# Kernel optimization log

Hardware: AMD Instinct MI355X
Metric: run time of the kernel (lower is better)

The kernel has to match this reference:

```python
import jax, jax.numpy as jnp
import numpy as np

T, B, E, H = 2048, 2, 1024, 16
Dh = E // H


def setup_inputs() -> dict:
    key = jax.random.key(0)
    ks = jax.random.split(key, 5)
    s = 0.02
    query = jax.random.normal(ks[0], (T, B, E), dtype=jnp.float32)
    Wq = jax.random.normal(ks[1], (E, E), dtype=jnp.float32) * s
    Wk = jax.random.normal(ks[2], (E, E), dtype=jnp.float32) * s
    Wv = jax.random.normal(ks[3], (E, E), dtype=jnp.float32) * s
    Wo = jax.random.normal(ks[4], (E, E), dtype=jnp.float32) * s
    bq = jnp.zeros((E,), jnp.float32)
    bk = jnp.zeros((E,), jnp.float32)
    bv = jnp.zeros((E,), jnp.float32)
    bo = jnp.zeros((E,), jnp.float32)
    # additive causal mask: 0 on/below diagonal, -inf above (standard fairseq usage)
    neg = jnp.finfo(jnp.float32).min
    attn_mask = jnp.where(jnp.triu(jnp.ones((T, T), jnp.bool_), k=1), neg, 0.0).astype(jnp.float32)
    return {"query": query, "Wq": Wq, "bq": bq, "Wk": Wk, "bk": bk,
            "Wv": Wv, "bv": bv, "Wo": Wo, "bo": bo, "attn_mask": attn_mask}


def reference(query, Wq, bq, Wk, bk, Wv, bv, Wo, bo, attn_mask):
    t, b, e = query.shape
    scale = Dh ** -0.5
    # self-attention projections (nn.Linear: x @ W.T + b)
    q = (query @ Wq.T + bq) * scale  # [T,B,E]
    k = query @ Wk.T + bk
    v = query @ Wv.T + bv
    # [T, B*H, Dh] -> [B*H, T, Dh]
    q = q.reshape(t, b * H, Dh).transpose(1, 0, 2)
    k = k.reshape(t, b * H, Dh).transpose(1, 0, 2)
    v = v.reshape(t, b * H, Dh).transpose(1, 0, 2)
    # explicit bmm -> softmax -> bmm (materializes [B*H, T, T])
    attn_weights = jnp.einsum('btd,bsd->bts', q, k) + attn_mask[None, :, :]
    attn_probs = jax.nn.softmax(attn_weights, axis=-1)
    attn = jnp.einsum('bts,bsd->btd', attn_probs, v)  # [B*H, T, Dh]
    attn = attn.transpose(1, 0, 2).reshape(t, b, e)  # [T,B,E]
    out = attn @ Wo.T + bo
    return out
```

## Files before the change

kernel.cpp:

```cpp
#include <hip/hip_runtime.h>


typedef __attribute__((ext_vector_type(8))) short   s16x8;
typedef __attribute__((ext_vector_type(4))) float   f32x4;
typedef __attribute__((ext_vector_type(2))) __fp16  f16x2;
typedef __attribute__((ext_vector_type(4))) __fp16  f16x4;

#define MFMA16(a, b, c) __builtin_amdgcn_mfma_f32_16x16x32_bf16((a), (b), (c), 0, 0, 0)
#define MFMApv(a, b, c) __builtin_amdgcn_mfma_f32_16x16x16f16((a), (b), (c), 0, 0, 0)

static __device__ __forceinline__ unsigned short f2bf(float f) {
    unsigned u = __float_as_uint(f);
    unsigned r = u + 0x7fffu + ((u >> 16) & 1u);
    return (unsigned short)(r >> 16);
}

static __device__ __forceinline__ void gl2lds16(const void* g, void* l) {
    __builtin_amdgcn_global_load_lds(
        (const __attribute__((address_space(1))) unsigned int*)g,
        (__attribute__((address_space(3))) unsigned int*)l, 16, 0, 0);
}

__global__ __launch_bounds__(256) void cvt_all(const float* __restrict__ query,
                                               const float* __restrict__ w0,
                                               const float* __restrict__ w1,
                                               const float* __restrict__ w2,
                                               const float* __restrict__ w3,
                                               unsigned short* __restrict__ Xb,
                                               unsigned short* __restrict__ Wcat) {
    const int bx = blockIdx.x;
    if (bx < 4096) {
        const int i = threadIdx.x;
        const float4 f = reinterpret_cast<const float4*>(query + (size_t)bx * 1024)[i];
        ushort4 u;
        u.x = f2bf(f.x); u.y = f2bf(f.y); u.z = f2bf(f.z); u.w = f2bf(f.w);
        const int mrow = (bx & 1) * 2048 + (bx >> 1);
        reinterpret_cast<ushort4*>(Xb + (size_t)mrow * 1024)[i] = u;
    } else {
        const int j   = bx - 4096;
        const int sel = j >> 10;
        const int i   = (j & 1023) * 256 + threadIdx.x;
        const float* src = (sel == 0) ? w0 : (sel == 1) ? w1 : (sel == 2) ? w2 : w3;
        const float4 f = reinterpret_cast<const float4*>(src)[i];
        ushort4 u;
        u.x = f2bf(f.x); u.y = f2bf(f.y); u.z = f2bf(f.z); u.w = f2bf(f.w);
        reinterpret_cast<ushort4*>(Wcat + (size_t)sel * 1048576)[i] = u;
    }
}

__global__ __launch_bounds__(256) void gemm_qkv(const unsigned short* __restrict__ A,
                                                const unsigned short* __restrict__ W,
                                                const float* __restrict__ b0,
                                                const float* __restrict__ b1,
                                                const float* __restrict__ b2,
                                                unsigned short* __restrict__ outQK,
                                                __fp16* __restrict__ outV) {
    __shared__ __align__(16) unsigned short smem[16384];
    unsigned short* Al = smem;
    unsigned short* Bl = smem + 8192;

    const int tid  = threadIdx.x;
    const int w    = tid >> 6;
    const int lane = tid & 63;
    const int quad = lane >> 4;
    const int c    = lane & 15;
    const int wm   = w >> 1;
    const int wn   = w & 1;

    const int id   = blockIdx.x;
    const int xcd  = id & 7;
    const int slot = id >> 3;
    const int m0 = (xcd * 4 + (slot & 3)) * 128;
    const int n0 = (slot >> 2) * 128;

    f32x4 acc[4][4];
    #pragma unroll
    for (int mi = 0; mi < 4; ++mi)
        #pragma unroll
        for (int ni = 0; ni < 4; ++ni) acc[mi][ni] = (f32x4){0.f, 0.f, 0.f, 0.f};

    const int srow = tid >> 3;
    const int g    = (tid & 7) ^ (srow & 7);
    const unsigned short* aG = A + (size_t)(m0 + srow) * 1024 + g * 8;
    const unsigned short* wG = W + (size_t)(n0 + srow) * 1024 + g * 8;
    const int loff = tid * 8;

    const int cs = (c & 7);

    for (int kk = 0; kk < 16; ++kk) {
        const int k0 = kk * 64;
        __syncthreads();
        #pragma unroll
        for (int i = 0; i < 4; ++i) {
            gl2lds16(aG + k0 + i * 32 * 1024, &Al[loff + i * 2048]);
            gl2lds16(wG + k0 + i * 32 * 1024, &Bl[loff + i * 2048]);
        }
        __syncthreads();

        s16x8 af[4][2], bf[4][2];
        #pragma unroll
        for (int mi = 0; mi < 4; ++mi) {
            const int row = (wm * 64 + mi * 16 + c) * 64;
            af[mi][0] = *reinterpret_cast<const s16x8*>(&Al[row + ((quad ^ cs) << 3)]);
            af[mi][1] = *reinterpret_cast<const s16x8*>(&Al[row + (((4 + quad) ^ cs) << 3)]);
        }
        #pragma unroll
        for (int ni = 0; ni < 4; ++ni) {
            const int row = (wn * 64 + ni * 16 + c) * 64;
            bf[ni][0] = *reinterpret_cast<const s16x8*>(&Bl[row + ((quad ^ cs) << 3)]);
            bf[ni][1] = *reinterpret_cast<const s16x8*>(&Bl[row + (((4 + quad) ^ cs) << 3)]);
        }
        #pragma unroll
        for (int mi = 0; mi < 4; ++mi)
            #pragma unroll
            for (int ni = 0; ni < 4; ++ni) {
                acc[mi][ni] = MFMA16(af[mi][0], bf[ni][0], acc[mi][ni]);
                acc[mi][ni] = MFMA16(af[mi][1], bf[ni][1], acc[mi][ni]);
            }
    }

    const int sel = n0 >> 10;
    if (sel < 2) {
        const float scale = (sel == 0) ? 0.18033688011112042f : 1.0f;
        const float* bias = (sel == 0) ? b0 : b1;
        #pragma unroll
        for (int ni = 0; ni < 4; ++ni) {
            const int n = n0 + wn * 64 + ni * 16 + c;
            const float bval = bias[n & 1023];
            #pragma unroll
            for (int mi = 0; mi < 4; ++mi)
                #pragma unroll
                for (int r = 0; r < 4; ++r) {
                    const int m = m0 + wm * 64 + mi * 16 + quad * 4 + r;
                    outQK[(size_t)m * 2048 + n] = f2bf((acc[mi][ni][r] + bval) * scale);
                }
        }
    } else {
        __syncthreads();
        #pragma unroll
        for (int ni = 0; ni < 4; ++ni) {
            const int n = wn * 64 + ni * 16 + c;
            const float bval = b2[(n0 - 2048) + n];
            #pragma unroll
            for (int mi = 0; mi < 4; ++mi) {
                const int m = wm * 64 + mi * 16 + quad * 4;
                const f16x2 lo = __builtin_amdgcn_cvt_pkrtz(acc[mi][ni][0] + bval,
                                                            acc[mi][ni][1] + bval);
                const f16x2 hi = __builtin_amdgcn_cvt_pkrtz(acc[mi][ni][2] + bval,
                                                            acc[mi][ni][3] + bval);
                uint2 st;
                st.x = __builtin_bit_cast(unsigned int, lo);
                st.y = __builtin_bit_cast(unsigned int, hi);
                const int phys = n * 128 + (((m >> 3) ^ (n & 15)) << 3) + (m & 7);
                *reinterpret_cast<uint2*>(&smem[phys]) = st;
            }
        }
        __syncthreads();
        const int n = tid >> 1;
        const int vcol = (n0 - 2048) + n;
        const int bb = m0 >> 11, tbase = m0 & 2047;
        __fp16* vdst = outV + ((size_t)((bb * 16 + (vcol >> 6)) * 64 + (vcol & 63))) * 2048 + tbase;
        #pragma unroll
        for (int j = 0; j < 8; ++j) {
            const int lc = (tid & 1) * 8 + j;
            const int phys = n * 128 + ((lc ^ (n & 15)) << 3);
            *reinterpret_cast<uint4*>(vdst + lc * 8) =
                *reinterpret_cast<const uint4*>(&smem[phys]);
        }
    }
}

__global__ __launch_bounds__(256) void gemm_out(const unsigned short* __restrict__ A,
                                                const unsigned short* __restrict__ W,
                                                const float* __restrict__ bias,
                                                float* __restrict__ outF) {
    __shared__ __align__(16) unsigned short Al[64 * 64];
    __shared__ __align__(16) unsigned short Bl[128 * 64];

    const int tid  = threadIdx.x;
    const int w    = tid >> 6;
    const int lane = tid & 63;
    const int quad = lane >> 4;
    const int c    = lane & 15;

    const int id   = blockIdx.x;
    const int xcd  = id & 7;
    const int slot = id >> 3;
    const int m0 = (xcd * 8 + (slot & 7)) * 64;
    const int n0 = (slot >> 3) * 128;

    f32x4 acc[8];
    #pragma unroll
    for (int ni = 0; ni < 8; ++ni) acc[ni] = (f32x4){0.f, 0.f, 0.f, 0.f};

    const int srow = tid >> 3;
    const int g    = (tid & 7) ^ (srow & 7);
    const unsigned short* aG = A + (size_t)(m0 + srow) * 1024 + g * 8;
    const unsigned short* wG = W + (size_t)(n0 + srow) * 1024 + g * 8;
    const int loff = tid * 8;

    const int cs = (c & 7);

    for (int kk = 0; kk < 16; ++kk) {
        const int k0 = kk * 64;
        __syncthreads();
        gl2lds16(aG + k0,             &Al[loff]);
        gl2lds16(aG + k0 + 32 * 1024, &Al[loff + 2048]);
        #pragma unroll
        for (int i = 0; i < 4; ++i)
            gl2lds16(wG + k0 + i * 32 * 1024, &Bl[loff + i * 2048]);
        __syncthreads();

        const int arow = (w * 16 + c) * 64;
        const s16x8 af0 = *reinterpret_cast<const s16x8*>(&Al[arow + ((quad ^ cs) << 3)]);
        const s16x8 af1 = *reinterpret_cast<const s16x8*>(&Al[arow + (((4 + quad) ^ cs) << 3)]);
        #pragma unroll
        for (int ni = 0; ni < 8; ++ni) {
            const int brow = (ni * 16 + c) * 64;
            const s16x8 bf0 = *reinterpret_cast<const s16x8*>(&Bl[brow + ((quad ^ cs) << 3)]);
            const s16x8 bf1 = *reinterpret_cast<const s16x8*>(&Bl[brow + (((4 + quad) ^ cs) << 3)]);
            acc[ni] = MFMA16(af0, bf0, acc[ni]);
            acc[ni] = MFMA16(af1, bf1, acc[ni]);
        }
    }

    #pragma unroll
    for (int ni = 0; ni < 8; ++ni) {
        const int n = n0 + ni * 16 + c;
        const float bval = bias[n];
        const int m = m0 + w * 16 + quad * 4;
        const int bb = m >> 11, t = m & 2047;
        #pragma unroll
        for (int r = 0; r < 4; ++r)
            outF[(size_t)(2 * (t + r) + bb) * 1024 + n] = acc[ni][r] + bval;
    }
}

__global__ __launch_bounds__(256, 4) void attn_kernel(const unsigned short* __restrict__ QKb,
                                                      const __fp16* __restrict__ Vt,
                                                      unsigned short* __restrict__ Ob) {
    __shared__ unsigned short Kl[2][2][64][32];
    __shared__ __fp16 Vl[2][64][64];

    const int tid  = threadIdx.x;
    const int w    = tid >> 6;
    const int lane = tid & 63;
    const int quad = lane >> 4;
    const int c    = lane & 15;

    const int id = blockIdx.x;
    const int bh = (id & 7) * 4 + ((id >> 3) & 3);
    const int a  = 31 - (id >> 5);
    const int bB = bh >> 4, h = bh & 15;
    const int t0 = a * 64;
    const int trg = t0 + w * 16;
    const int nIt = a + 1;

    const unsigned short* qp = QKb + (size_t)(bB * 2048 + trg + c) * 2048 + h * 64 + quad * 8;
    const s16x8 aq0 = *reinterpret_cast<const s16x8*>(qp);
    const s16x8 aq1 = *reinterpret_cast<const s16x8*>(qp + 32);

    const int lr4 = lane >> 2, sl4 = lane & 3;
    const unsigned short* kSrc = QKb + (size_t)(bB * 2048 + w * 16 + lr4) * 2048
                                 + 1024 + h * 64 + (sl4 ^ ((lane >> 3) & 3)) * 8;
    const int vr8 = lane >> 3, sl8 = lane & 7;
    const __fp16* vSrcA = Vt + (size_t)(bh * 64 + w * 16 + vr8) * 2048 + (sl8 ^ vr8) * 8;
    const __fp16* vSrcB = vSrcA + (size_t)8 * 2048;

    f32x4 acc[4];
    float l = 0.f;
    #pragma unroll
    for (int dt = 0; dt < 4; ++dt) acc[dt] = (f32x4){0.f, 0.f, 0.f, 0.f};

    const int kswz = (quad ^ ((c >> 1) & 3)) * 8;

    {
        gl2lds16(kSrc,      &Kl[0][0][w * 16 + lr4][sl4 * 8]);
        gl2lds16(kSrc + 32, &Kl[0][1][w * 16 + lr4][sl4 * 8]);
        gl2lds16(vSrcA,     &Vl[0][w * 16 + vr8][sl8 * 8]);
        gl2lds16(vSrcB,     &Vl[0][w * 16 + 8 + vr8][sl8 * 8]);
    }

    for (int it = 0; it < nIt; ++it) {
        const int buf = it & 1;
        __syncthreads();
        if (it + 1 < nIt) {
            const size_t s1 = (size_t)(it + 1) * 64;
            const int nb = buf ^ 1;
            gl2lds16(kSrc + s1 * 2048,      &Kl[nb][0][w * 16 + lr4][sl4 * 8]);
            gl2lds16(kSrc + s1 * 2048 + 32, &Kl[nb][1][w * 16 + lr4][sl4 * 8]);
            gl2lds16(vSrcA + s1,            &Vl[nb][w * 16 + vr8][sl8 * 8]);
            gl2lds16(vSrcB + s1,            &Vl[nb][w * 16 + 8 + vr8][sl8 * 8]);
        }

        s16x8 kf[4][2];
        #pragma unroll
        for (int ns = 0; ns < 4; ++ns) {
            kf[ns][0] = *reinterpret_cast<const s16x8*>(&Kl[buf][0][ns * 16 + c][kswz]);
            kf[ns][1] = *reinterpret_cast<const s16x8*>(&Kl[buf][1][ns * 16 + c][kswz]);
        }
        f16x4 vf[4][4];
        #pragma unroll
        for (int dt = 0; dt < 4; ++dt)
            #pragma unroll
            for (int ch = 0; ch < 4; ++ch) {
                const int phys = ((2 * ch + (quad >> 1)) ^ (c & 7)) * 8 + (quad & 1) * 4;
                vf[dt][ch] = *reinterpret_cast<const f16x4*>(&Vl[buf][dt * 16 + c][phys]);
            }

        const int s0 = it * 64;
        const bool diag = (it == a);
        f32x4 sT[4];
        #pragma unroll
        for (int ns = 0; ns < 4; ++ns) {
            f32x4 z = (f32x4){0.f, 0.f, 0.f, 0.f};
            z = MFMA16(kf[ns][0], aq0, z);
            sT[ns] = MFMA16(kf[ns][1], aq1, z);
        }
        f16x4 pf[4];
        float lp = 0.f;
        #pragma unroll
        for (int ns = 0; ns < 4; ++ns) {
            float pv[4];
            #pragma unroll
            for (int r = 0; r < 4; ++r) pv[r] = exp2f(sT[ns][r]);
            if (diag) {
                const int sb = s0 + ns * 16 + quad * 4;
                const int qg = trg + c;
                #pragma unroll
                for (int r = 0; r < 4; ++r) if (sb + r > qg) pv[r] = 0.f;
            }
            lp += (pv[0] + pv[1]) + (pv[2] + pv[3]);
            const f16x2 lo = __builtin_amdgcn_cvt_pkrtz(pv[0], pv[1]);
            const f16x2 hi = __builtin_amdgcn_cvt_pkrtz(pv[2], pv[3]);
            pf[ns] = __builtin_shufflevector(lo, hi, 0, 1, 2, 3);
        }
        l += lp;
        #pragma unroll
        for (int dt = 0; dt < 4; ++dt)
            #pragma unroll
            for (int ns = 0; ns < 4; ++ns)
                acc[dt] = MFMApv(vf[dt][ns], pf[ns], acc[dt]);
    }

    float lv = l;
    lv += __shfl_xor(lv, 16);
    lv += __shfl_xor(lv, 32);
    const float inv = 1.0f / lv;
    const size_t base = (size_t)(bB * 2048 + trg + c) * 1024 + h * 64;
    #pragma unroll
    for (int dt = 0; dt < 4; ++dt) {
        const unsigned u0 = (unsigned)f2bf(acc[dt][0] * inv)
                          | ((unsigned)f2bf(acc[dt][1] * inv) << 16);
        const unsigned u1 = (unsigned)f2bf(acc[dt][2] * inv)
                          | ((unsigned)f2bf(acc[dt][3] * inv) << 16);
        uint2 st; st.x = u0; st.y = u1;
        *reinterpret_cast<uint2*>(Ob + base + dt * 16 + quad * 4) = st;
    }
}

extern "C" void kernel_launch(void* const* d_in, const int* in_sizes, int n_in,
                              void* d_out, int out_size, void* d_ws, size_t ws_size,
                              hipStream_t stream) {
    const float* query = (const float*)d_in[0];
    const float* Wq    = (const float*)d_in[1];
    const float* bq    = (const float*)d_in[2];
    const float* Wk    = (const float*)d_in[3];
    const float* bk    = (const float*)d_in[4];
    const float* Wv    = (const float*)d_in[5];
    const float* bv    = (const float*)d_in[6];
    const float* Wo    = (const float*)d_in[7];
    const float* bo    = (const float*)d_in[8];

    float* out = (float*)d_out;

    unsigned short* ws    = (unsigned short*)d_ws;
    unsigned short* Xbf   = ws;
    unsigned short* Wcat  = Xbf  + (size_t)4096 * 1024;
    unsigned short* QKb   = Wcat + (size_t)4 * 1024 * 1024;
    __fp16*         Vtw   = (__fp16*)(QKb + (size_t)4096 * 2048);
    unsigned short* attnb = (unsigned short*)(Vtw + (size_t)32 * 64 * 2048);

    cvt_all<<<8192, 256, 0, stream>>>(query, Wq, Wk, Wv, Wo, Xbf, Wcat);

    gemm_qkv<<<768, 256, 0, stream>>>(Xbf, Wcat, bq, bk, bv, QKb, Vtw);

    attn_kernel<<<1024, 256, 0, stream>>>(QKb, Vtw, attnb);

    gemm_out<<<512, 256, 0, stream>>>(attnb, Wcat + (size_t)3 * 1024 * 1024,
                                      bo, out);
}
```

Measured before the change: 199.9 us.

## Enlarge QKV GEMM tiles to 256x256 with 8 waves and double-buffered LDS pipeline

```diff
diff --git a/kernel.cpp b/kernel.cpp
--- a/kernel.cpp
+++ b/kernel.cpp
@@ -48,34 +48,32 @@
     }
 }
 
-__global__ __launch_bounds__(256) void gemm_qkv(const unsigned short* __restrict__ A,
-                                                const unsigned short* __restrict__ W,
-                                                const float* __restrict__ b0,
-                                                const float* __restrict__ b1,
-                                                const float* __restrict__ b2,
-                                                unsigned short* __restrict__ outQK,
-                                                __fp16* __restrict__ outV) {
-    __shared__ __align__(16) unsigned short smem[16384];
-    unsigned short* Al = smem;
-    unsigned short* Bl = smem + 8192;
+__global__ __launch_bounds__(512, 2) void gemm_qkv(const unsigned short* __restrict__ A,
+                                                   const unsigned short* __restrict__ W,
+                                                   const float* __restrict__ b0,
+                                                   const float* __restrict__ b1,
+                                                   const float* __restrict__ b2,
+                                                   unsigned short* __restrict__ outQK,
+                                                   __fp16* __restrict__ outV) {
+    __shared__ __align__(16) unsigned short smem[65536];
 
     const int tid  = threadIdx.x;
     const int w    = tid >> 6;
     const int lane = tid & 63;
     const int quad = lane >> 4;
     const int c    = lane & 15;
-    const int wm   = w >> 1;
-    const int wn   = w & 1;
+    const int wm   = w >> 2;
+    const int wn   = w & 3;
 
     const int id   = blockIdx.x;
     const int xcd  = id & 7;
     const int slot = id >> 3;
-    const int m0 = (xcd * 4 + (slot & 3)) * 128;
-    const int n0 = (slot >> 2) * 128;
-
-    f32x4 acc[4][4];
+    const int m0 = (xcd * 2 + (slot & 1)) * 256;
+    const int n0 = (slot >> 1) * 256;
+
+    f32x4 acc[8][4];
     #pragma unroll
-    for (int mi = 0; mi < 4; ++mi)
+    for (int mi = 0; mi < 8; ++mi)
         #pragma unroll
         for (int ni = 0; ni < 4; ++ni) acc[mi][ni] = (f32x4){0.f, 0.f, 0.f, 0.f};
 
@@ -85,87 +83,166 @@
     const unsigned short* wG = W + (size_t)(n0 + srow) * 1024 + g * 8;
     const int loff = tid * 8;
 
-    const int cs = (c & 7);
-
-    for (int kk = 0; kk < 16; ++kk) {
-        const int k0 = kk * 64;
-        __syncthreads();
-        #pragma unroll
-        for (int i = 0; i < 4; ++i) {
-            gl2lds16(aG + k0 + i * 32 * 1024, &Al[loff + i * 2048]);
-            gl2lds16(wG + k0 + i * 32 * 1024, &Bl[loff + i * 2048]);
-        }
-        __syncthreads();
-
-        s16x8 af[4][2], bf[4][2];
+#define STA(buf, u, k0) gl2lds16(aG + (k0) + (u) * 65536, &smem[(buf) * 32768 + (u) * 4096 + loff])
+#define STB(buf, u, k0) gl2lds16(wG + (k0) + (u) * 65536, &smem[(buf) * 32768 + 16384 + (u) * 4096 + loff])
+
+    STB(0, 0, 0); STB(0, 1, 0); STB(0, 2, 0); STB(0, 3, 0);
+    STA(0, 0, 0); STA(0, 2, 0); STA(0, 1, 0); STA(0, 3, 0);
+    asm volatile("s_waitcnt vmcnt(2)" ::: "memory");
+    asm volatile("s_barrier" ::: "memory");
+
+    const int cs  = c & 7;
+    const int ch0 = (quad ^ cs) << 3;
+    const int ch1 = ((4 + quad) ^ cs) << 3;
+
+    s16x8 af[4][2], bl[2][2], bh[2][2];
+
+    #pragma unroll 1
+    for (int t = 0; t < 16; ++t) {
+        const unsigned short* Al = &smem[(t & 1) * 32768];
+        const unsigned short* Bl = Al + 16384;
+        const int  nb   = (t & 1) ^ 1;
+        const int  kn   = (t + 1) * 64;
+        const bool more = (t < 15);
+
         #pragma unroll
         for (int mi = 0; mi < 4; ++mi) {
-            const int row = (wm * 64 + mi * 16 + c) * 64;
-            af[mi][0] = *reinterpret_cast<const s16x8*>(&Al[row + ((quad ^ cs) << 3)]);
-            af[mi][1] = *reinterpret_cast<const s16x8*>(&Al[row + (((4 + quad) ^ cs) << 3)]);
-        }
-        #pragma unroll
-        for (int ni = 0; ni < 4; ++ni) {
+            const int row = (wm * 128 + mi * 16 + c) * 64;
+            af[mi][0] = *reinterpret_cast<const s16x8*>(&Al[row + ch0]);
+            af[mi][1] = *reinterpret_cast<const s16x8*>(&Al[row + ch1]);
+        }
+        #pragma unroll
+        for (int ni = 0; ni < 2; ++ni) {
             const int row = (wn * 64 + ni * 16 + c) * 64;
-            bf[ni][0] = *reinterpret_cast<const s16x8*>(&Bl[row + ((quad ^ cs) << 3)]);
-            bf[ni][1] = *reinterpret_cast<const s16x8*>(&Bl[row + (((4 + quad) ^ cs) << 3)]);
-        }
+            bl[ni][0] = *reinterpret_cast<const s16x8*>(&Bl[row + ch0]);
+            bl[ni][1] = *reinterpret_cast<const s16x8*>(&Bl[row + ch1]);
+        }
+        if (more) { STB(nb, 0, kn); STB(nb, 1, kn); }
+        asm volatile("s_barrier" ::: "memory");
+        __builtin_amdgcn_s_setprio(1);
         #pragma unroll
         for (int mi = 0; mi < 4; ++mi)
             #pragma unroll
-            for (int ni = 0; ni < 4; ++ni) {
-                acc[mi][ni] = MFMA16(af[mi][0], bf[ni][0], acc[mi][ni]);
-                acc[mi][ni] = MFMA16(af[mi][1], bf[ni][1], acc[mi][ni]);
-            }
-    }
-
-    const int sel = n0 >> 10;
-    if (sel < 2) {
-        const float scale = (sel == 0) ? 0.18033688011112042f : 1.0f;
-        const float* bias = (sel == 0) ? b0 : b1;
+            for (int ni = 0; ni < 2; ++ni) {
+                acc[mi][ni] = MFMA16(af[mi][0], bl[ni][0], acc[mi][ni]);
+                acc[mi][ni] = MFMA16(af[mi][1], bl[ni][1], acc[mi][ni]);
+            }
+        __builtin_amdgcn_s_setprio(0);
+        asm volatile("s_barrier" ::: "memory");
+
+        #pragma unroll
+        for (int ni = 0; ni < 2; ++ni) {
+            const int row = (wn * 64 + (2 + ni) * 16 + c) * 64;
+            bh[ni][0] = *reinterpret_cast<const s16x8*>(&Bl[row + ch0]);
+            bh[ni][1] = *reinterpret_cast<const s16x8*>(&Bl[row + ch1]);
+        }
+        if (more) { STB(nb, 2, kn); STB(nb, 3, kn); }
+        asm volatile("s_barrier" ::: "memory");
+        __builtin_amdgcn_s_setprio(1);
+        #pragma unroll
+        for (int mi = 0; mi < 4; ++mi)
+            #pragma unroll
+            for (int ni = 0; ni < 2; ++ni) {
+                acc[mi][2 + ni] = MFMA16(af[mi][0], bh[ni][0], acc[mi][2 + ni]);
+                acc[mi][2 + ni] = MFMA16(af[mi][1], bh[ni][1], acc[mi][2 + ni]);
+            }
+        __builtin_amdgcn_s_setprio(0);
+        if (more) asm volatile("s_waitcnt vmcnt(4)" ::: "memory");
+        else      asm volatile("s_waitcnt vmcnt(0)" ::: "memory");
+        asm volatile("s_barrier" ::: "memory");
+
+        #pragma unroll
+        for (int mi = 0; mi < 4; ++mi) {
+            const int row = (wm * 128 + (4 + mi) * 16 + c) * 64;
+            af[mi][0] = *reinterpret_cast<const s16x8*>(&Al[row + ch0]);
+            af[mi][1] = *reinterpret_cast<const s16x8*>(&Al[row + ch1]);
+        }
+        if (more) { STA(nb, 0, kn); STA(nb, 2, kn); }
+        asm volatile("s_barrier" ::: "memory");
+        __builtin_amdgcn_s_setprio(1);
+        #pragma unroll
+        for (int mi = 0; mi < 4; ++mi)
+            #pragma unroll
+            for (int ni = 0; ni < 2; ++ni) {
+                acc[4 + mi][ni] = MFMA16(af[mi][0], bl[ni][0], acc[4 + mi][ni]);
+                acc[4 + mi][ni] = MFMA16(af[mi][1], bl[ni][1], acc[4 + mi][ni]);
+            }
+        __builtin_amdgcn_s_setprio(0);
+        asm volatile("s_barrier" ::: "memory");
+
+        if (more) { STA(nb, 1, kn); STA(nb, 3, kn); }
+        asm volatile("s_barrier" ::: "memory");
+        __builtin_amdgcn_s_setprio(1);
+        #pragma unroll
+        for (int mi = 0; mi < 4; ++mi)
+            #pragma unroll
+            for (int ni = 0; ni < 2; ++ni) {
+                acc[4 + mi][2 + ni] = MFMA16(af[mi][0], bh[ni][0], acc[4 + mi][2 + ni]);
+                acc[4 + mi][2 + ni] = MFMA16(af[mi][1], bh[ni][1], acc[4 + mi][2 + ni]);
+            }
+        __builtin_amdgcn_s_setprio(0);
+        if (more) asm volatile("s_waitcnt vmcnt(2)" ::: "memory");
+        asm volatile("s_barrier" ::: "memory");
+    }
+#undef STA
+#undef STB
+
+    if (n0 < 2048) {
+        const float scale = (n0 < 1024) ? 0.18033688011112042f : 1.0f;
+        const float* bias = (n0 < 1024) ? b0 : b1;
         #pragma unroll
         for (int ni = 0; ni < 4; ++ni) {
             const int n = n0 + wn * 64 + ni * 16 + c;
             const float bval = bias[n & 1023];
             #pragma unroll
-            for (int mi = 0; mi < 4; ++mi)
+            for (int mi = 0; mi < 8; ++mi)
                 #pragma unroll
                 for (int r = 0; r < 4; ++r) {
-                    const int m = m0 + wm * 64 + mi * 16 + quad * 4 + r;
+                    const int m = m0 + wm * 128 + mi * 16 + quad * 4 + r;
                     outQK[(size_t)m * 2048 + n] = f2bf((acc[mi][ni][r] + bval) * scale);
                 }
         }
     } else {
-        __syncthreads();
-        #pragma unroll
-        for (int ni = 0; ni < 4; ++ni) {
-            const int n = wn * 64 + ni * 16 + c;
-            const float bval = b2[(n0 - 2048) + n];
-            #pragma unroll
-            for (int mi = 0; mi < 4; ++mi) {
-                const int m = wm * 64 + mi * 16 + quad * 4;
-                const f16x2 lo = __builtin_amdgcn_cvt_pkrtz(acc[mi][ni][0] + bval,
-                                                            acc[mi][ni][1] + bval);
-                const f16x2 hi = __builtin_amdgcn_cvt_pkrtz(acc[mi][ni][2] + bval,
-                                                            acc[mi][ni][3] + bval);
-                uint2 st;
-                st.x = __builtin_bit_cast(unsigned int, lo);
-                st.y = __builtin_bit_cast(unsigned int, hi);
-                const int phys = n * 128 + (((m >> 3) ^ (n & 15)) << 3) + (m & 7);
-                *reinterpret_cast<uint2*>(&smem[phys]) = st;
-            }
-        }
-        __syncthreads();
-        const int n = tid >> 1;
-        const int vcol = (n0 - 2048) + n;
-        const int bb = m0 >> 11, tbase = m0 & 2047;
-        __fp16* vdst = outV + ((size_t)((bb * 16 + (vcol >> 6)) * 64 + (vcol & 63))) * 2048 + tbase;
-        #pragma unroll
-        for (int j = 0; j < 8; ++j) {
-            const int lc = (tid & 1) * 8 + j;
-            const int phys = n * 128 + ((lc ^ (n & 15)) << 3);
-            *reinterpret_cast<uint4*>(vdst + lc * 8) =
-                *reinterpret_cast<const uint4*>(&smem[phys]);
+        __fp16* lds16 = reinterpret_cast<__fp16*>(smem);
+        #pragma unroll 1
+        for (int tn = 0; tn < 2; ++tn) {
+            __syncthreads();
+            if ((wn >> 1) == tn) {
+                #pragma unroll
+                for (int ni = 0; ni < 4; ++ni) {
+                    const int nLoc = (wn & 1) * 64 + ni * 16 + c;
+                    const float bval = b2[(n0 - 2048) + tn * 128 + nLoc];
+                    #pragma unroll
+                    for (int mi = 0; mi < 8; ++mi) {
+                        const int mLoc = mi * 16 + quad * 4;
+                        const f16x2 lo = __builtin_amdgcn_cvt_pkrtz(acc[mi][ni][0] + bval,
+                                                                    acc[mi][ni][1] + bval);
+                        const f16x2 hi = __builtin_amdgcn_cvt_pkrtz(acc[mi][ni][2] + bval,
+                                                                    acc[mi][ni][3] + bval);
+                        uint2 st;
+                        st.x = __builtin_bit_cast(unsigned int, lo);
+                        st.y = __builtin_bit_cast(unsigned int, hi);
+                        const int phys = wm * 16384 + nLoc * 128 +
+                                         (((mLoc >> 3) ^ (nLoc & 15)) << 3) + (mLoc & 7);
+                        *reinterpret_cast<uint2*>(&lds16[phys]) = st;
+                    }
+                }
+            }
+            __syncthreads();
+            const int np   = tid >> 1;
+            const int rg   = np >> 7;
+            const int nLoc = np & 127;
+            const int vcol = (n0 - 2048) + tn * 128 + nLoc;
+            const int bb = m0 >> 11;
+            const int tbase = (m0 & 2047) + rg * 128;
+            __fp16* vdst = outV + ((size_t)((bb * 16 + (vcol >> 6)) * 64 + (vcol & 63))) * 2048 + tbase;
+            #pragma unroll
+            for (int j = 0; j < 8; ++j) {
+                const int lc = (tid & 1) * 8 + j;
+                *reinterpret_cast<uint4*>(vdst + lc * 8) =
+                    *reinterpret_cast<const uint4*>(
+                        &lds16[rg * 16384 + nLoc * 128 + ((lc ^ (nLoc & 15)) << 3)]);
+            }
         }
     }
 }
@@ -383,7 +460,7 @@
 
     cvt_all<<<8192, 256, 0, stream>>>(query, Wq, Wk, Wv, Wo, Xbf, Wcat);
 
-    gemm_qkv<<<768, 256, 0, stream>>>(Xbf, Wcat, bq, bk, bv, QKb, Vtw);
+    gemm_qkv<<<192, 512, 0, stream>>>(Xbf, Wcat, bq, bk, bv, QKb, Vtw);
 
     attn_kernel<<<1024, 256, 0, stream>>>(QKb, Vtw, attnb);
 
```

Measured after the change: 192.8 us. 3.6% less time.
